# Optimization experiments

Measured on AMD Instinct MI355X. Metric: run time of the kernel, lower is better.

## Reference

```python
import jax, jax.numpy as jnp
import numpy as np

B, T, D, DFF, H, W = 2, 2048, 1024, 4096, 16, 512
HD = D // H
EPS = 1e-6
NEG = jnp.float32(-1e30)


def _rms(x, w):
    return x * jax.lax.rsqrt(jnp.mean(x * x, axis=-1, keepdims=True) + EPS) * w


def setup_inputs() -> dict:
    key = jax.random.key(0)
    ks = jax.random.split(key, 12)
    g = lambda k, shape, std: jax.random.normal(k, shape, jnp.float32) * std
    return {
        "x": jax.random.normal(ks[0], (B, T, D), jnp.float32),
        "retrieval_context": jax.random.normal(ks[1], (B, D), jnp.float32),
        "norm1_w": jnp.ones((D,), jnp.float32),
        "qkv_w": g(ks[2], (3 * D, D), 0.02),
        "qkv_b": jnp.zeros((3 * D,), jnp.float32),
        "proj_w": g(ks[3], (D, D), 0.02),
        "proj_b": jnp.zeros((D,), jnp.float32),
        "gate_w": g(ks[4], (3, D), 0.01),
        "gate_b": jnp.zeros((3,), jnp.float32),
        "ret_w": g(ks[5], (D, D), 0.01),
        "norm2_w": jnp.ones((D,), jnp.float32),
        "ffn_gate_w": g(ks[6], (DFF, D), 0.02),
        "ffn_up_w": g(ks[7], (DFF, D), 0.02),
        "ffn_down_w": g(ks[8], (D, DFF), 0.02),
    }


def reference(x, retrieval_context, norm1_w, qkv_w, qkv_b, proj_w, proj_b,
              gate_w, gate_b, ret_w, norm2_w, ffn_gate_w, ffn_up_w, ffn_down_w):
    # pre-norm
    h = _rms(x, norm1_w)  # (B,T,D)
    # qkv projection, split into heads
    qkv = h @ qkv_w.T + qkv_b  # (B,T,3D)
    q, k, v = jnp.split(qkv, 3, axis=-1)
    to_heads = lambda t: t.reshape(B, T, H, HD).transpose(0, 2, 1, 3)  # (B,H,T,HD)
    q, k, v = to_heads(q), to_heads(k), to_heads(v)
    # sliding-window causal mask: attend to j in [i-W+1, i]
    idx = jnp.arange(T)
    win = (idx[:, None] >= idx[None, :]) & (idx[:, None] - idx[None, :] < W)  # (T,T)
    scores = jnp.einsum("bhqd,bhkd->bhqk", q, k) / np.sqrt(HD).astype(np.float32)
    scores = jnp.where(win, scores, NEG)
    attn = jax.nn.softmax(scores, axis=-1)
    attn_out = jnp.einsum("bhqk,bhkd->bhqd", attn, v)  # (B,H,T,HD)
    attn_out = attn_out.transpose(0, 2, 1, 3).reshape(B, T, D)
    attn_out = attn_out @ proj_w.T + proj_b
    # retrieval stream (TRN disabled -> zeros, gate channel 1 hard-masked)
    ret_out = (retrieval_context @ ret_w.T)[:, None, :]  # (B,1,D) broadcast over T
    gate_logits = h @ gate_w.T + gate_b  # (B,T,3)
    gate_logits = gate_logits.at[:, :, 1].set(-1e9)  # enable_trn=False
    gates = jax.nn.softmax(gate_logits, axis=-1)
    mixed = gates[:, :, 0:1] * attn_out + gates[:, :, 2:3] * ret_out
    x = x + mixed
    # SwiGLU FFN
    h2 = _rms(x, norm2_w)
    ffn = (jax.nn.silu(h2 @ ffn_gate_w.T) * (h2 @ ffn_up_w.T)) @ ffn_down_w.T
    return x + ffn
```

## Files before the change

kernel.cpp:

```cpp
#include <hip/hip_runtime.h>
#include <hip/hip_bf16.h>

typedef __bf16 bf16_t;
typedef __bf16 bf16x8 __attribute__((ext_vector_type(8)));
typedef __bf16 bf16x4v __attribute__((ext_vector_type(4)));
typedef float f32x4 __attribute__((ext_vector_type(4)));

static constexpr int Bn = 2, Tn = 2048, Dn = 1024, DFFn = 4096, Hn = 16, HDn = 64, Wn = 512;
static constexpr int Mn = Bn * Tn;

#define MFMA16(a, b, c) __builtin_amdgcn_mfma_f32_16x16x32_bf16(a, b, c, 0, 0, 0)

typedef __attribute__((address_space(3))) void lds_void;
typedef const __attribute__((address_space(1))) void gbl_void;

__global__ __launch_bounds__(256) void cvt_f32_bf16_kernel(const float4* __restrict__ src,
                                                           bf16x4v* __restrict__ dst, int n4) {
  int i = blockIdx.x * 256 + threadIdx.x;
  if (i < n4) {
    float4 v = src[i];
    bf16x4v o;
    o[0] = (bf16_t)v.x; o[1] = (bf16_t)v.y; o[2] = (bf16_t)v.z; o[3] = (bf16_t)v.w;
    dst[i] = o;
  }
}

__device__ __forceinline__ float blockReduceSum(float v, float* sbuf) {
#pragma unroll
  for (int off = 32; off > 0; off >>= 1) v += __shfl_down(v, off, 64);
  int lane = threadIdx.x & 63, wid = threadIdx.x >> 6;
  __syncthreads();
  if (lane == 0) sbuf[wid] = v;
  __syncthreads();
  return sbuf[0] + sbuf[1] + sbuf[2] + sbuf[3];
}

template <bool GATE>
__global__ __launch_bounds__(256) void rmsnorm_kernel(const float* __restrict__ x,
                                                      const float* __restrict__ w,
                                                      bf16_t* __restrict__ out,
                                                      const float* __restrict__ gw,
                                                      const float* __restrict__ gb,
                                                      float* __restrict__ gates) {
  __shared__ float sbuf[4];
  int row = blockIdx.x, tid = threadIdx.x;
  const float4* xr = (const float4*)(x + (long)row * Dn);
  float4 v = xr[tid];
  float ss = v.x * v.x + v.y * v.y + v.z * v.z + v.w * v.w;
  ss = blockReduceSum(ss, sbuf);
  float rms = rsqrtf(ss * (1.0f / Dn) + 1e-6f);
  float4 wv = ((const float4*)w)[tid];
  float h0 = v.x * rms * wv.x, h1 = v.y * rms * wv.y;
  float h2 = v.z * rms * wv.z, h3 = v.w * rms * wv.w;
  bf16x4v o;
  o[0] = (bf16_t)h0; o[1] = (bf16_t)h1; o[2] = (bf16_t)h2; o[3] = (bf16_t)h3;
  ((bf16x4v*)(out + (long)row * Dn))[tid] = o;
  if (GATE) {
    float4 g0v = ((const float4*)gw)[tid];
    float4 g2v = ((const float4*)(gw + 2 * Dn))[tid];
    float l0 = h0 * g0v.x + h1 * g0v.y + h2 * g0v.z + h3 * g0v.w;
    float l2 = h0 * g2v.x + h1 * g2v.y + h2 * g2v.z + h3 * g2v.w;
    l0 = blockReduceSum(l0, sbuf);
    l2 = blockReduceSum(l2, sbuf);
    if (tid == 0) {
      l0 += gb[0];
      l2 += gb[2];
      float mx = fmaxf(l0, l2);
      float e0 = __expf(l0 - mx), e2 = __expf(l2 - mx);
      float inv = 1.0f / (e0 + e2);
      gates[2 * row] = e0 * inv;
      gates[2 * row + 1] = e2 * inv;
    }
  }
}

__global__ __launch_bounds__(512, 2) void gemm256_kernel(const bf16_t* __restrict__ Ag,
                                                         const bf16_t* __restrict__ Wt, int K,
                                                         int N, const float* __restrict__ bias,
                                                         bf16_t* __restrict__ outb) {
  __shared__ bf16_t lds2[65536];
  const int tid = threadIdx.x;
  const int wid = tid >> 6, lane = tid & 63;
  const int wr = wid >> 2, wc = wid & 3;
  const int m0 = blockIdx.y * 256, n0 = blockIdx.x * 256;
  const int lr = lane & 15, lg = lane >> 4;
  const int lterm = (lr * 32 + lg * 8) ^ (((lr >> 3) & 1) << 4);
  const int colsw = (lane & 3) * 8 ^ (((lane >> 5) & 1) << 4);
  const int NT = K >> 6;

  auto stageA = [&](int buf, int half, int t) {
#pragma unroll
    for (int q = 0; q < 2; q++) {
      int s = q * 8 + wid, s_r = s >> 1, s_c = s & 1;
      const bf16_t* src =
          Ag + (long)(m0 + half * 128 + s_r * 16 + (lane >> 2)) * K + (long)t * 64 + s_c * 32 + colsw;
      bf16_t* dst = &lds2[buf * 32768 + (half * 8 + s_r) * 1024 + s_c * 512];
      __builtin_amdgcn_global_load_lds((gbl_void*)src, (lds_void*)dst, 16, 0, 0);
    }
  };
  auto stageB = [&](int buf, int half, int t) {
#pragma unroll
    for (int q = 0; q < 2; q++) {
      int s = q * 8 + wid, s_r = s >> 1, s_c = s & 1;
      const bf16_t* src =
          Wt + (long)(n0 + half * 128 + s_r * 16 + (lane >> 2)) * K + (long)t * 64 + s_c * 32 + colsw;
      bf16_t* dst = &lds2[buf * 32768 + 16384 + (half * 8 + s_r) * 1024 + s_c * 512];
      __builtin_amdgcn_global_load_lds((gbl_void*)src, (lds_void*)dst, 16, 0, 0);
    }
  };

  f32x4 acc[8][4];
#pragma unroll
  for (int i = 0; i < 8; i++)
#pragma unroll
    for (int j = 0; j < 4; j++) acc[i][j] = (f32x4){0.f, 0.f, 0.f, 0.f};

  stageB(0, 0, 0);
  stageB(0, 1, 0);
  stageA(0, 0, 0);
  stageA(0, 1, 0);
  if (NT > 1) {
    stageB(1, 0, 1);
    stageB(1, 1, 1);
    asm volatile("s_waitcnt vmcnt(4)" ::: "memory");
  } else {
    asm volatile("s_waitcnt vmcnt(0)" ::: "memory");
  }
  __builtin_amdgcn_sched_barrier(0);
  __builtin_amdgcn_s_barrier();

#define LDA(mi, ks) (*(const bf16x8*)&lds2[ca + ((wr << 3) + (mi)) * 1024 + (ks)*512 + lterm])
#define LDB(ni, ks) (*(const bf16x8*)&lds2[cb + ((wc << 2) + (ni)) * 1024 + (ks)*512 + lterm])

#define GPHASE(mi0, ...)                                                                  \
  do {                                                                                    \
    bf16x8 a0k0 = LDA(mi0, 0), a0k1 = LDA(mi0, 1);                                        \
    bf16x8 a1k0 = LDA((mi0) + 1, 0), a1k1 = LDA((mi0) + 1, 1);                            \
    __VA_ARGS__;                                                                          \
    __builtin_amdgcn_s_barrier();                                                         \
    asm volatile("s_waitcnt lgkmcnt(0)" ::: "memory");                                    \
    __builtin_amdgcn_sched_barrier(0);                                                    \
    __builtin_amdgcn_s_setprio(1);                                                        \
    _Pragma("unroll") for (int ni = 0; ni < 4; ni++) {                                    \
      acc[mi0][ni] = MFMA16(a0k0, bfr[ni][0], acc[mi0][ni]);                              \
      acc[mi0][ni] = MFMA16(a0k1, bfr[ni][1], acc[mi0][ni]);                              \
      acc[(mi0) + 1][ni] = MFMA16(a1k0, bfr[ni][0], acc[(mi0) + 1][ni]);                  \
      acc[(mi0) + 1][ni] = MFMA16(a1k1, bfr[ni][1], acc[(mi0) + 1][ni]);                  \
    }                                                                                     \
    __builtin_amdgcn_s_setprio(0);                                                        \
    __builtin_amdgcn_s_barrier();                                                         \
  } while (0)

#define GTILE(t, cur)                                                                     \
  do {                                                                                    \
    const int ca = (cur)*32768, cb = ca + 16384;                                          \
    bf16x8 bfr[4][2];                                                                     \
    _Pragma("unroll") for (int ni = 0; ni < 4; ni++) {                                    \
      bfr[ni][0] = LDB(ni, 0);                                                            \
      bfr[ni][1] = LDB(ni, 1);                                                            \
    }                                                                                     \
    GPHASE(0, {                                                                           \
      if ((t) + 1 < NT) {                                                                 \
        stageA(1 - (cur), 0, (t) + 1);                                                    \
        stageA(1 - (cur), 1, (t) + 1);                                                    \
      }                                                                                   \
    });                                                                                   \
    GPHASE(2, {                                                                           \
      if ((t) + 2 < NT) stageB((cur), 0, (t) + 2);                                        \
    });                                                                                   \
    GPHASE(4, {                                                                           \
      if ((t) + 2 < NT) stageB((cur), 1, (t) + 2);                                        \
    });                                                                                   \
    GPHASE(6, {});                                                                        \
    if ((t) + 1 < NT) {                                                                   \
      if ((t) + 2 < NT)                                                                   \
        asm volatile("s_waitcnt vmcnt(4)" ::: "memory");                                  \
      else                                                                                \
        asm volatile("s_waitcnt vmcnt(0)" ::: "memory");                                  \
      __builtin_amdgcn_sched_barrier(0);                                                  \
      __builtin_amdgcn_s_barrier();                                                       \
    }                                                                                     \
  } while (0)

  for (int t = 0; t < NT; t += 2) {
    GTILE(t, 0);
    GTILE(t + 1, 1);
  }

#pragma unroll
  for (int mi = 0; mi < 8; mi++) {
#pragma unroll
    for (int rr = 0; rr < 4; rr++) {
      long r = m0 + wr * 128 + mi * 16 + lg * 4 + rr;
#pragma unroll
      for (int ni = 0; ni < 4; ni++) {
        int c = n0 + wc * 64 + ni * 16 + lr;
        float v = acc[mi][ni][rr];
        if (bias) v += bias[c];
        outb[r * N + c] = (bf16_t)v;
      }
    }
  }
#undef LDA
#undef LDB
#undef GPHASE
#undef GTILE
}

template <int EPI>
__global__ __launch_bounds__(256) void gemm128_kernel(const bf16_t* __restrict__ A,
                                                      const bf16_t* __restrict__ Wt, int K, int N,
                                                      const float* __restrict__ bias,
                                                      float* __restrict__ outf,
                                                      const float* __restrict__ gates,
                                                      const float* __restrict__ ret,
                                                      const float* __restrict__ resid) {
  __shared__ bf16_t lds[32768];
  const int tid = threadIdx.x, wid = tid >> 6, lane = tid & 63;
  const int wr = wid >> 1, wc = wid & 1;
  const int m0 = blockIdx.y * 128, n0 = blockIdx.x * 128;
  const int lr = lane & 15, lg = lane >> 4;
  const int lterm = (lr * 32 + lg * 8) ^ (((lr >> 3) & 1) << 4);
  const int colsw = (lane & 3) * 8 ^ (((lane >> 5) & 1) << 4);
  const int NT = K >> 6;

  auto stage = [&](int buf, int t) {
#pragma unroll
    for (int q = 0; q < 8; q++) {
      int c = wid * 8 + q;
      int isB = c >> 4;
      int cc = c & 15;
      int s_r = cc >> 1, s_c = cc & 1;
      const bf16_t* base = isB ? Wt + (long)(n0 + s_r * 16 + (lane >> 2)) * K
                               : A + (long)(m0 + s_r * 16 + (lane >> 2)) * K;
      const bf16_t* src = base + (long)t * 64 + s_c * 32 + colsw;
      bf16_t* dst = &lds[buf * 16384 + isB * 8192 + (s_r * 2 + s_c) * 512];
      __builtin_amdgcn_global_load_lds((gbl_void*)src, (lds_void*)dst, 16, 0, 0);
    }
  };

  f32x4 acc[4][4];
#pragma unroll
  for (int i = 0; i < 4; i++)
#pragma unroll
    for (int j = 0; j < 4; j++) acc[i][j] = (f32x4){0.f, 0.f, 0.f, 0.f};

  stage(0, 0);
  __syncthreads();

  for (int t = 0; t < NT; t++) {
    const int cur = t & 1;
    if (t + 1 < NT) stage(cur ^ 1, t + 1);
    const int ab = cur * 16384;
#pragma unroll
    for (int ks = 0; ks < 2; ks++) {
      bf16x8 af[4], bfv[4];
#pragma unroll
      for (int mi = 0; mi < 4; mi++)
        af[mi] = *(const bf16x8*)&lds[ab + ((wr * 4 + mi) * 2 + ks) * 512 + lterm];
#pragma unroll
      for (int ni = 0; ni < 4; ni++)
        bfv[ni] = *(const bf16x8*)&lds[ab + 8192 + ((wc * 4 + ni) * 2 + ks) * 512 + lterm];
#pragma unroll
      for (int mi = 0; mi < 4; mi++)
#pragma unroll
        for (int ni = 0; ni < 4; ni++) acc[mi][ni] = MFMA16(af[mi], bfv[ni], acc[mi][ni]);
    }
    if (t + 1 < NT) __syncthreads();
  }

#pragma unroll
  for (int mi = 0; mi < 4; mi++) {
#pragma unroll
    for (int rr2 = 0; rr2 < 4; rr2++) {
      int r = m0 + wr * 64 + mi * 16 + lg * 4 + rr2;
      float g0 = 0.f, g2 = 0.f;
      const float* retb = nullptr;
      if (EPI == 2) {
        g0 = gates[2 * r];
        g2 = gates[2 * r + 1];
        retb = ret + ((r >> 11) << 10);
      }
#pragma unroll
      for (int ni = 0; ni < 4; ni++) {
        int c = n0 + wc * 64 + ni * 16 + lr;
        float v = acc[mi][ni][rr2];
        long idx = (long)r * N + c;
        if (EPI == 2) {
          outf[idx] = resid[idx] + g0 * (v + bias[c]) + g2 * retb[c];
        } else {
          outf[idx] = resid[idx] + v;
        }
      }
    }
  }
}

__global__ __launch_bounds__(256) void retproj_kernel(const float* __restrict__ rc,
                                                      const float* __restrict__ rw,
                                                      float* __restrict__ out) {
  int gw = blockIdx.x * 4 + (threadIdx.x >> 6);
  int lane = threadIdx.x & 63;
  int b = gw >> 10, n = gw & 1023;
  float v = 0.f;
  for (int k = lane; k < Dn; k += 64) v += rc[b * Dn + k] * rw[(long)n * Dn + k];
#pragma unroll
  for (int off = 32; off > 0; off >>= 1) v += __shfl_down(v, off, 64);
  if (lane == 0) out[gw] = v;
}

__global__ __launch_bounds__(256) void attn_kernel(const bf16_t* __restrict__ qkv,
                                                   bf16_t* __restrict__ out) {
  __shared__ bf16_t psh[4][512];
  const int tid = threadIdx.x, w = tid >> 6, lane = tid & 63;
  const int qb = blockIdx.x, bh = blockIdx.y;
  const int b = bh >> 4, h = bh & 15;
  const int qw0 = qb * 64 + w * 16;
  const bf16_t* base = qkv + (long)b * Tn * 3072 + h * 64;
  const bf16_t* kb = base + Dn;
  const bf16_t* vb = base + 2 * Dn;
  const int lr = lane & 15, lg = lane >> 4;

  bf16x8 aq0 = *(const bf16x8*)(base + (long)(qw0 + lr) * 3072 + lg * 8);
  bf16x8 aq1 = *(const bf16x8*)(base + (long)(qw0 + lr) * 3072 + lg * 8 + 32);

  float m_run[4], l_run[4];
  f32x4 accv[4];
#pragma unroll
  for (int r = 0; r < 4; r++) { m_run[r] = -1e30f; l_run[r] = 0.f; }
#pragma unroll
  for (int c = 0; c < 4; c++) accv[c] = (f32x4){0.f, 0.f, 0.f, 0.f};

  int j_lo = qw0 - (Wn - 1);
  if (j_lo < 0) j_lo = 0;
  j_lo &= ~31;
  const int j_hi = qw0 + 15;

  for (int j0 = j_lo; j0 <= j_hi; j0 += 32) {
    f32x4 s[2];
#pragma unroll
    for (int hh = 0; hh < 2; hh++) {
      const bf16_t* kr = kb + (long)(j0 + hh * 16 + lr) * 3072 + lg * 8;
      bf16x8 k0 = *(const bf16x8*)kr;
      bf16x8 k1 = *(const bf16x8*)(kr + 32);
      f32x4 z = (f32x4){0.f, 0.f, 0.f, 0.f};
      z = MFMA16(aq0, k0, z);
      z = MFMA16(aq1, k1, z);
      s[hh] = z;
    }
    float mt[4];
#pragma unroll
    for (int r = 0; r < 4; r++) {
      int q = qw0 + lg * 4 + r;
      int c0 = j0 + lr, c1 = j0 + 16 + lr;
      float s0 = (q >= c0 && (q - c0) < Wn) ? s[0][r] * 0.125f : -1e30f;
      float s1 = (q >= c1 && (q - c1) < Wn) ? s[1][r] * 0.125f : -1e30f;
      s[0][r] = s0;
      s[1][r] = s1;
      mt[r] = fmaxf(s0, s1);
    }
#pragma unroll
    for (int off = 1; off < 16; off <<= 1)
#pragma unroll
      for (int r = 0; r < 4; r++) mt[r] = fmaxf(mt[r], __shfl_xor(mt[r], off, 64));
    float rs[4];
#pragma unroll
    for (int r = 0; r < 4; r++) {
      float nm = fmaxf(m_run[r], mt[r]);
      float alpha = __expf(m_run[r] - nm);
      m_run[r] = nm;
      float p0 = __expf(s[0][r] - nm);
      float p1 = __expf(s[1][r] - nm);
      psh[w][(lg * 4 + r) * 32 + lr] = (bf16_t)p0;
      psh[w][(lg * 4 + r) * 32 + 16 + lr] = (bf16_t)p1;
      rs[r] = p0 + p1;
      l_run[r] *= alpha;
#pragma unroll
      for (int c = 0; c < 4; c++) accv[c][r] *= alpha;
    }
#pragma unroll
    for (int off = 1; off < 16; off <<= 1)
#pragma unroll
      for (int r = 0; r < 4; r++) rs[r] += __shfl_xor(rs[r], off, 64);
#pragma unroll
    for (int r = 0; r < 4; r++) l_run[r] += rs[r];

    bf16x8 ap = *(const bf16x8*)&psh[w][lr * 32 + lg * 8];
#pragma unroll
    for (int c = 0; c < 4; c++) {
      bf16x8 bv;
#pragma unroll
      for (int jj = 0; jj < 8; jj++) bv[jj] = vb[(long)(j0 + lg * 8 + jj) * 3072 + c * 16 + lr];
      accv[c] = MFMA16(ap, bv, accv[c]);
    }
  }
#pragma unroll
  for (int r = 0; r < 4; r++) {
    float inv = 1.0f / l_run[r];
    long orow = ((long)b * Tn + qw0 + lg * 4 + r) * Dn + h * 64;
#pragma unroll
    for (int c = 0; c < 4; c++) out[orow + c * 16 + lr] = (bf16_t)(accv[c][r] * inv);
  }
}

__global__ __launch_bounds__(256) void silu_mul_kernel(const bf16_t* __restrict__ gu,
                                                       bf16_t* __restrict__ act) {
  int m = blockIdx.y;
  int j0 = (blockIdx.x * 256 + threadIdx.x) * 8;
  bf16x8 g = *(const bf16x8*)(gu + (long)m * (2 * DFFn) + j0);
  bf16x8 u = *(const bf16x8*)(gu + (long)m * (2 * DFFn) + DFFn + j0);
  bf16x8 o;
#pragma unroll
  for (int i = 0; i < 8; i++) {
    float gf = (float)g[i], uf = (float)u[i];
    float sf = gf / (1.0f + __expf(-gf));
    o[i] = (bf16_t)(sf * uf);
  }
  *(bf16x8*)(act + (long)m * DFFn + j0) = o;
}

extern "C" void kernel_launch(void* const* d_in, const int* in_sizes, int n_in, void* d_out,
                              int out_size, void* d_ws, size_t ws_size, hipStream_t stream) {
  const float* x = (const float*)d_in[0];
  const float* rc = (const float*)d_in[1];
  const float* n1w = (const float*)d_in[2];
  const float* qkv_w = (const float*)d_in[3];
  const float* qkv_b = (const float*)d_in[4];
  const float* proj_w = (const float*)d_in[5];
  const float* proj_b = (const float*)d_in[6];
  const float* gate_w = (const float*)d_in[7];
  const float* gate_b = (const float*)d_in[8];
  const float* ret_w = (const float*)d_in[9];
  const float* n2w = (const float*)d_in[10];
  const float* fgw = (const float*)d_in[11];
  const float* fuw = (const float*)d_in[12];
  const float* fdw = (const float*)d_in[13];
  float* out = (float*)d_out;

  char* ws = (char*)d_ws;
  size_t off = 0;
  auto alloc = [&](size_t bytes) {
    char* p = ws + off;
    off += (bytes + 255) & ~(size_t)255;
    return p;
  };
  bf16_t* wqkv = (bf16_t*)alloc(3072l * 1024 * 2);
  bf16_t* wproj = (bf16_t*)alloc(1024l * 1024 * 2);
  bf16_t* wgup = (bf16_t*)alloc(8192l * 1024 * 2);
  bf16_t* wdown = (bf16_t*)alloc(1024l * 4096 * 2);
  bf16_t* h1 = (bf16_t*)alloc((long)Mn * 1024 * 2);
  bf16_t* h2 = (bf16_t*)alloc((long)Mn * 1024 * 2);
  bf16_t* qkvb = (bf16_t*)alloc((long)Mn * 3072 * 2);
  bf16_t* attnb = (bf16_t*)alloc((long)Mn * 1024 * 2);
  bf16_t* gupo = (bf16_t*)alloc((long)Mn * 8192 * 2);
  bf16_t* actb = (bf16_t*)alloc((long)Mn * 4096 * 2);
  float* gates = (float*)alloc((long)Mn * 2 * 4);
  float* retb = (float*)alloc(2048 * 4);
  float* xmid = (float*)alloc((long)Mn * 1024 * 4);

  cvt_f32_bf16_kernel<<<3072, 256, 0, stream>>>((const float4*)qkv_w, (bf16x4v*)wqkv, 786432);
  cvt_f32_bf16_kernel<<<1024, 256, 0, stream>>>((const float4*)proj_w, (bf16x4v*)wproj, 262144);
  cvt_f32_bf16_kernel<<<4096, 256, 0, stream>>>((const float4*)fgw, (bf16x4v*)wgup, 1048576);
  cvt_f32_bf16_kernel<<<4096, 256, 0, stream>>>((const float4*)fuw, (bf16x4v*)(wgup + 4194304),
                                                1048576);
  cvt_f32_bf16_kernel<<<4096, 256, 0, stream>>>((const float4*)fdw, (bf16x4v*)wdown, 1048576);

  rmsnorm_kernel<true><<<Mn, 256, 0, stream>>>(x, n1w, h1, gate_w, gate_b, gates);
  gemm256_kernel<<<dim3(12, 16), 512, 0, stream>>>(h1, wqkv, 1024, 3072, qkv_b, qkvb);
  retproj_kernel<<<512, 256, 0, stream>>>(rc, ret_w, retb);
  attn_kernel<<<dim3(32, 32), 256, 0, stream>>>(qkvb, attnb);
  gemm128_kernel<2><<<dim3(8, 32), 256, 0, stream>>>(attnb, wproj, 1024, 1024, proj_b, xmid, gates,
                                                     retb, x);
  rmsnorm_kernel<false><<<Mn, 256, 0, stream>>>(xmid, n2w, h2, nullptr, nullptr, nullptr);
  gemm256_kernel<<<dim3(32, 16), 512, 0, stream>>>(h2, wgup, 1024, 8192, nullptr, gupo);
  silu_mul_kernel<<<dim3(2, 4096), 256, 0, stream>>>(gupo, actb);
  gemm128_kernel<3><<<dim3(8, 32), 256, 0, stream>>>(actb, wdown, 4096, 1024, nullptr, out,
                                                     nullptr, nullptr, xmid);
}
```

Before: 431.5 us.

## Fuse SiLU-gating into gate/up GEMM epilogue via interleaved weight rows

Interleaves the gate and up FFN weight rows during bf16 conversion so adjacent output columns hold matching gate/up pairs. The gate/up GEMM epilogue then uses a lane shuffle to pair them and writes silu(g)*u directly, which removes the separate silu_mul kernel and the round trip of the 4096x8192 bf16 intermediate through memory. Each epilogue write is now half-width and strided, so stores may coalesce less well.

```diff
diff --git a/kernel.cpp b/kernel.cpp
--- a/kernel.cpp
+++ b/kernel.cpp
@@ -23,6 +23,19 @@
     o[0] = (bf16_t)v.x; o[1] = (bf16_t)v.y; o[2] = (bf16_t)v.z; o[3] = (bf16_t)v.w;
     dst[i] = o;
   }
+}
+
+__global__ __launch_bounds__(256) void cvt_interleave_kernel(const float4* __restrict__ g,
+                                                             const float4* __restrict__ u,
+                                                             bf16x4v* __restrict__ dst) {
+  int i = blockIdx.x * 256 + threadIdx.x;
+  int j = i >> 8, c4 = i & 255;
+  float4 vg = g[i], vu = u[i];
+  bf16x4v og, ou;
+  og[0] = (bf16_t)vg.x; og[1] = (bf16_t)vg.y; og[2] = (bf16_t)vg.z; og[3] = (bf16_t)vg.w;
+  ou[0] = (bf16_t)vu.x; ou[1] = (bf16_t)vu.y; ou[2] = (bf16_t)vu.z; ou[3] = (bf16_t)vu.w;
+  dst[(2 * j) * 256 + c4] = og;
+  dst[(2 * j + 1) * 256 + c4] = ou;
 }
 
 __device__ __forceinline__ float blockReduceSum(float v, float* sbuf) {
@@ -74,6 +87,7 @@
   }
 }
 
+template <int EPI>
 __global__ __launch_bounds__(512, 2) void gemm256_kernel(const bf16_t* __restrict__ Ag,
                                                          const bf16_t* __restrict__ Wt, int K,
                                                          int N, const float* __restrict__ bias,
@@ -178,7 +192,7 @@
       else                                                                                \
         asm volatile("s_waitcnt vmcnt(0)" ::: "memory");                                  \
       __builtin_amdgcn_sched_barrier(0);                                                  \
-      __builtin_amdgcn_s_barrier();                                                       \
+      __builtin_amdgcn_s_barrier();                                                      \
     }                                                                                     \
   } while (0)
 
@@ -196,8 +210,16 @@
       for (int ni = 0; ni < 4; ni++) {
         int c = n0 + wc * 64 + ni * 16 + lr;
         float v = acc[mi][ni][rr];
-        if (bias) v += bias[c];
-        outb[r * N + c] = (bf16_t)v;
+        if (EPI == 0) {
+          if (bias) v += bias[c];
+          outb[r * N + c] = (bf16_t)v;
+        } else {
+          float p = __shfl_xor(v, 1, 64);
+          if (!(lr & 1)) {
+            float s = v / (1.0f + __expf(-v));
+            outb[r * (N >> 1) + (c >> 1)] = (bf16_t)(s * p);
+          }
+        }
       }
     }
   }
@@ -401,22 +423,6 @@
 #pragma unroll
     for (int c = 0; c < 4; c++) out[orow + c * 16 + lr] = (bf16_t)(accv[c][r] * inv);
   }
-}
-
-__global__ __launch_bounds__(256) void silu_mul_kernel(const bf16_t* __restrict__ gu,
-                                                       bf16_t* __restrict__ act) {
-  int m = blockIdx.y;
-  int j0 = (blockIdx.x * 256 + threadIdx.x) * 8;
-  bf16x8 g = *(const bf16x8*)(gu + (long)m * (2 * DFFn) + j0);
-  bf16x8 u = *(const bf16x8*)(gu + (long)m * (2 * DFFn) + DFFn + j0);
-  bf16x8 o;
-#pragma unroll
-  for (int i = 0; i < 8; i++) {
-    float gf = (float)g[i], uf = (float)u[i];
-    float sf = gf / (1.0f + __expf(-gf));
-    o[i] = (bf16_t)(sf * uf);
-  }
-  *(bf16x8*)(act + (long)m * DFFn + j0) = o;
 }
 
 extern "C" void kernel_launch(void* const* d_in, const int* in_sizes, int n_in, void* d_out,
@@ -452,7 +458,6 @@
   bf16_t* h2 = (bf16_t*)alloc((long)Mn * 1024 * 2);
   bf16_t* qkvb = (bf16_t*)alloc((long)Mn * 3072 * 2);
   bf16_t* attnb = (bf16_t*)alloc((long)Mn * 1024 * 2);
-  bf16_t* gupo = (bf16_t*)alloc((long)Mn * 8192 * 2);
   bf16_t* actb = (bf16_t*)alloc((long)Mn * 4096 * 2);
   float* gates = (float*)alloc((long)Mn * 2 * 4);
   float* retb = (float*)alloc(2048 * 4);
@@ -460,20 +465,18 @@
 
   cvt_f32_bf16_kernel<<<3072, 256, 0, stream>>>((const float4*)qkv_w, (bf16x4v*)wqkv, 786432);
   cvt_f32_bf16_kernel<<<1024, 256, 0, stream>>>((const float4*)proj_w, (bf16x4v*)wproj, 262144);
-  cvt_f32_bf16_kernel<<<4096, 256, 0, stream>>>((const float4*)fgw, (bf16x4v*)wgup, 1048576);
-  cvt_f32_bf16_kernel<<<4096, 256, 0, stream>>>((const float4*)fuw, (bf16x4v*)(wgup + 4194304),
-                                                1048576);
+  cvt_interleave_kernel<<<4096, 256, 0, stream>>>((const float4*)fgw, (const float4*)fuw,
+                                                  (bf16x4v*)wgup);
   cvt_f32_bf16_kernel<<<4096, 256, 0, stream>>>((const float4*)fdw, (bf16x4v*)wdown, 1048576);
 
   rmsnorm_kernel<true><<<Mn, 256, 0, stream>>>(x, n1w, h1, gate_w, gate_b, gates);
-  gemm256_kernel<<<dim3(12, 16), 512, 0, stream>>>(h1, wqkv, 1024, 3072, qkv_b, qkvb);
+  gemm256_kernel<0><<<dim3(12, 16), 512, 0, stream>>>(h1, wqkv, 1024, 3072, qkv_b, qkvb);
   retproj_kernel<<<512, 256, 0, stream>>>(rc, ret_w, retb);
   attn_kernel<<<dim3(32, 32), 256, 0, stream>>>(qkvb, attnb);
   gemm128_kernel<2><<<dim3(8, 32), 256, 0, stream>>>(attnb, wproj, 1024, 1024, proj_b, xmid, gates,
                                                      retb, x);
   rmsnorm_kernel<false><<<Mn, 256, 0, stream>>>(xmid, n2w, h2, nullptr, nullptr, nullptr);
-  gemm256_kernel<<<dim3(32, 16), 512, 0, stream>>>(h2, wgup, 1024, 8192, nullptr, gupo);
-  silu_mul_kernel<<<dim3(2, 4096), 256, 0, stream>>>(gupo, actb);
+  gemm256_kernel<1><<<dim3(32, 16), 512, 0, stream>>>(h2, wgup, 1024, 8192, nullptr, actb);
   gemm128_kernel<3><<<dim3(8, 32), 256, 0, stream>>>(actb, wdown, 4096, 1024, nullptr, out,
                                                      nullptr, nullptr, xmid);
 }
```

Result: no change. 429.6 us (-0.4%).
